# Performance work log

Hardware: AMD Instinct MI355X
Metric: run time of the kernel (lower is better)

## Reference

```python
import jax, jax.numpy as jnp
import numpy as np

TOP_K = 5
EPS = 1e-12

def _l2norm(x, axis=-1):
    n = jnp.sqrt(jnp.sum(x * x, axis=axis, keepdims=True))
    return x / jnp.maximum(n, EPS)

def setup_inputs() -> dict:
    key = jax.random.key(0)
    ks = jax.random.split(key, 6)
    B, S, D, N = 16, 2048, 512, 200000
    return {
        "hidden_states": jax.random.normal(ks[0], (B, S, D), dtype=jnp.float32),
        "doc_embeddings": jax.random.normal(ks[1], (N, D), dtype=jnp.float32),
        "W_q": jax.random.normal(ks[2], (D, D), dtype=jnp.float32) * 0.02,
        "b_q": jnp.zeros((D,), dtype=jnp.float32),
        "W_gate": jax.random.normal(ks[3], (D, 2 * D), dtype=jnp.float32) * 0.02,
        "b_gate": jnp.zeros((D,), dtype=jnp.float32),
    }

def reference(hidden_states, doc_embeddings, W_q, b_q, W_gate, b_gate):
    B, S, D = hidden_states.shape
    # set_doc_embeddings: cosine metric normalizes doc table once
    docs = _l2norm(doc_embeddings, axis=1)          # [N, D]
    # forward: mean-pool query, linear encode
    query = hidden_states.mean(axis=1)              # [B, D]
    query = query @ W_q.T + b_q                     # torch Linear: x @ W^T + b
    # cosine similarity scan over full corpus
    q = _l2norm(query, axis=1)                      # [B, D]
    scores_full = q @ docs.T                        # [B, N]  (memory-bound scan)
    top_scores, indices = jax.lax.top_k(scores_full, TOP_K)  # [B, K], [B, K]
    # fuse context (gate method)
    retrieved = docs[indices]                       # [B, K, D] gather
    weights = jax.nn.softmax(top_scores, axis=1)    # [B, K]
    context = jnp.einsum('bk,bkd->bd', weights, retrieved)   # [B, D]
    context_exp = jnp.broadcast_to(context[:, None, :], (B, S, D))
    combined = jnp.concatenate([hidden_states, context_exp], axis=-1)  # [B, S, 2D]
    gate = jax.nn.sigmoid(combined @ W_gate.T + b_gate)       # [B, S, D]
    fused = gate * hidden_states + (1.0 - gate) * context_exp
    return top_scores, indices, fused
```

## Files before the change

### kernel.cpp

```cpp
#include <hip/hip_runtime.h>
#include <hip/hip_bf16.h>
#include <math.h>

#define BB 16
#define SS 2048
#define DD 512
#define NDOCS 200000
#define TOPK 5
#define EPSN 1e-12f
#define NEG_INF (-3.0e38f)

#define TILE_N 128
#define KC 64
#define NCHUNK (DD / KC)
#define NBLK3 ((NDOCS + TILE_N - 1) / TILE_N)

typedef short s16x8 __attribute__((ext_vector_type(8)));
typedef float f32x4 __attribute__((ext_vector_type(4)));

__device__ __forceinline__ short f2bf(float f) {
    __bf16 b = (__bf16)f;
    short s;
    __builtin_memcpy(&s, &b, 2);
    return s;
}

__device__ __forceinline__ void gload_lds16(const void* g, void* l) {
    __builtin_amdgcn_global_load_lds(
        (const __attribute__((address_space(1))) void*)g,
        (__attribute__((address_space(3))) void*)l, 16, 0, 0);
}

__global__ __launch_bounds__(128) void k1_mean_partial(
    const float* __restrict__ hs, float* __restrict__ partial) {
    int b = blockIdx.y, sc = blockIdx.x;
    int t = threadIdx.x;
    const float4* src = (const float4*)(hs + (size_t)(b * SS + sc * 64) * DD);
    float4 acc = {0.f, 0.f, 0.f, 0.f};
    for (int s = 0; s < 64; ++s) {
        float4 v = src[(size_t)s * 128 + t];
        acc.x += v.x; acc.y += v.y; acc.z += v.z; acc.w += v.w;
    }
    ((float4*)partial)[(size_t)(sc * BB + b) * 128 + t] = acc;
}

__global__ __launch_bounds__(128) void k1b_mean_reduce(
    const float* __restrict__ partial, float* __restrict__ mean) {
    int b = blockIdx.y, jc = blockIdx.x;
    int j = jc * 128 + threadIdx.x;
    float s = 0.f;
    for (int c = 0; c < 32; ++c) s += partial[(size_t)(c * BB + b) * DD + j];
    mean[(size_t)b * DD + j] = s * (1.0f / 2048.0f);
}

__global__ __launch_bounds__(256) void k2a_q_gemv(
    const float* __restrict__ mean, const float* __restrict__ Wq,
    const float* __restrict__ bq, float* __restrict__ qtmp) {
    int b = blockIdx.y, jc = blockIdx.x;
    int t = threadIdx.x;
    int r = t >> 4, c = t & 15;
    int row = jc * 16 + r;
    const float4* wr = (const float4*)(Wq + (size_t)row * DD);
    const float4* mv = (const float4*)(mean + (size_t)b * DD);
    float acc = 0.f;
#pragma unroll
    for (int it = 0; it < 8; ++it) {
        int k4 = c + it * 16;
        float4 w = wr[k4], m = mv[k4];
        acc = fmaf(w.x, m.x, acc); acc = fmaf(w.y, m.y, acc);
        acc = fmaf(w.z, m.z, acc); acc = fmaf(w.w, m.w, acc);
    }
#pragma unroll
    for (int m = 1; m < 16; m <<= 1) acc += __shfl_xor(acc, m);
    if (c == 0) qtmp[(size_t)b * DD + row] = acc + bq[row];
}

__global__ __launch_bounds__(256) void k2b_q_norm(
    const float* __restrict__ qtmp, float* __restrict__ qv) {
    int b = blockIdx.x, t = threadIdx.x;
    __shared__ float red[4];
    float a0 = qtmp[(size_t)b * DD + t];
    float a1 = qtmp[(size_t)b * DD + t + 256];
    float ss = a0 * a0 + a1 * a1;
#pragma unroll
    for (int m = 1; m < 64; m <<= 1) ss += __shfl_xor(ss, m);
    if ((t & 63) == 0) red[t >> 6] = ss;
    __syncthreads();
    float inv = 1.0f / fmaxf(sqrtf(red[0] + red[1] + red[2] + red[3]), EPSN);
    qv[(size_t)b * DD + t] = a0 * inv;
    qv[(size_t)b * DD + t + 256] = a1 * inv;
}

__global__ __launch_bounds__(256) void k3_scores(
    const float* __restrict__ docs, const float* __restrict__ qv,
    float* __restrict__ cand_s, int* __restrict__ cand_i) {
    __shared__ float4 Et[2][TILE_N * 16];

    int t = threadIdx.x;
    int w = t >> 6, lane = t & 63;
    int ln = lane & 15, bg = lane >> 4;
    int blk = blockIdx.x;
    long tileBase = (long)blk * TILE_N;

    const float4* q4 = (const float4*)qv;

    auto stage = [&](int c, int buf) {
#pragma unroll
        for (int j = 0; j < 8; ++j) {
            int u = ((w * 8 + j) << 6) + lane;
            int n = u >> 4, slot = u & 15;
            int k4src = slot ^ (n & 15);
            long row = tileBase + n;
            if (row > NDOCS - 1) row = NDOCS - 1;
            const float* g = docs + row * (long)DD + c * KC + k4src * 4;
            gload_lds16(g, (void*)&Et[buf][(w * 8 + j) * 64]);
        }
    };

    float acc[2][4];
    float nrm[2];
#pragma unroll
    for (int i = 0; i < 2; ++i) {
        nrm[i] = 0.f;
#pragma unroll
        for (int j = 0; j < 4; ++j) acc[i][j] = 0.f;
    }

    stage(0, 0);
    for (int c = 0; c < NCHUNK; ++c) {
        __syncthreads();
        if (c + 1 < NCHUNK) stage(c + 1, (c + 1) & 1);
        const float4* Eb = &Et[c & 1][0];
        int c16 = c * 16;
#pragma unroll
        for (int k4 = 0; k4 < 16; ++k4) {
            float4 q0 = q4[(bg * 4 + 0) * 128 + c16 + k4];
            float4 q1 = q4[(bg * 4 + 1) * 128 + c16 + k4];
            float4 q2 = q4[(bg * 4 + 2) * 128 + c16 + k4];
            float4 q3 = q4[(bg * 4 + 3) * 128 + c16 + k4];
#pragma unroll
            for (int i = 0; i < 2; ++i) {
                int n = (w << 5) + ln + (i << 4);
                float4 e = Eb[(n << 4) + (k4 ^ (n & 15))];
                nrm[i]    = fmaf(e.x, e.x, fmaf(e.y, e.y, fmaf(e.z, e.z, fmaf(e.w, e.w, nrm[i]))));
                acc[i][0] = fmaf(e.x, q0.x, fmaf(e.y, q0.y, fmaf(e.z, q0.z, fmaf(e.w, q0.w, acc[i][0]))));
                acc[i][1] = fmaf(e.x, q1.x, fmaf(e.y, q1.y, fmaf(e.z, q1.z, fmaf(e.w, q1.w, acc[i][1]))));
                acc[i][2] = fmaf(e.x, q2.x, fmaf(e.y, q2.y, fmaf(e.z, q2.z, fmaf(e.w, q2.w, acc[i][2]))));
                acc[i][3] = fmaf(e.x, q3.x, fmaf(e.y, q3.y, fmaf(e.z, q3.z, fmaf(e.w, q3.w, acc[i][3]))));
            }
        }
    }

    float* Sb = (float*)&Et[0][0];
    __syncthreads();
#pragma unroll
    for (int i = 0; i < 2; ++i) {
        int n = (w << 5) + ln + (i << 4);
        float inv = 1.0f / fmaxf(sqrtf(nrm[i]), EPSN);
#pragma unroll
        for (int j = 0; j < 4; ++j)
            Sb[(bg * 4 + j) * TILE_N + n] = acc[i][j] * inv;
    }
    __syncthreads();

    for (int jj = 0; jj < 4; ++jj) {
        int b = w * 4 + jj;
        float v[2]; int nn[2];
#pragma unroll
        for (int m = 0; m < 2; ++m) {
            int n = lane + m * 64;
            nn[m] = n;
            v[m] = (tileBase + n < NDOCS) ? Sb[b * TILE_N + n] : NEG_INF;
        }
        for (int r = 0; r < TOPK; ++r) {
            float bv = v[0]; int bi = nn[0];
            if (v[1] > bv || (v[1] == bv && nn[1] < bi)) { bv = v[1]; bi = nn[1]; }
#pragma unroll
            for (int mm = 1; mm < 64; mm <<= 1) {
                float ov = __shfl_xor(bv, mm);
                int   oi = __shfl_xor(bi, mm);
                if (ov > bv || (ov == bv && oi < bi)) { bv = ov; bi = oi; }
            }
            if (lane == 0) {
                cand_s[((long)blk * BB + b) * TOPK + r] = bv;
                cand_i[((long)blk * BB + b) * TOPK + r] = (int)(tileBase + bi);
            }
#pragma unroll
            for (int m = 0; m < 2; ++m)
                if (nn[m] == bi) v[m] = NEG_INF;
        }
    }
}

__global__ __launch_bounds__(256) void k4a_topk_ctx(
    const float* __restrict__ docs, const float* __restrict__ cand_s,
    const int* __restrict__ cand_i, float* __restrict__ ctx,
    float* __restrict__ outp) {
    int b = blockIdx.x, t = threadIdx.x;
    __shared__ float sv[256];
    __shared__ int   si[256];
    __shared__ float topv[TOPK];
    __shared__ int   topi[TOPK];
    __shared__ float red[4];
    __shared__ float nrm5[TOPK];
    __shared__ float wts[TOPK];

    float lv[TOPK]; int li[TOPK];
#pragma unroll
    for (int r = 0; r < TOPK; ++r) { lv[r] = NEG_INF; li[r] = 0x7fffffff; }

    for (int j = t; j < NBLK3 * TOPK; j += 256) {
        int blk = j / TOPK, r = j - blk * TOPK;
        float s = cand_s[(long)blk * (BB * TOPK) + b * TOPK + r];
        int  di = cand_i[(long)blk * (BB * TOPK) + b * TOPK + r];
        if (s > lv[TOPK - 1] || (s == lv[TOPK - 1] && di < li[TOPK - 1])) {
            lv[TOPK - 1] = s; li[TOPK - 1] = di;
#pragma unroll
            for (int k = TOPK - 1; k > 0; --k) {
                if (lv[k] > lv[k - 1] || (lv[k] == lv[k - 1] && li[k] < li[k - 1])) {
                    float tv = lv[k]; lv[k] = lv[k - 1]; lv[k - 1] = tv;
                    int   ti = li[k]; li[k] = li[k - 1]; li[k - 1] = ti;
                }
            }
        }
    }

    int p = 0;
    for (int r = 0; r < TOPK; ++r) {
        float hv = (p < TOPK) ? lv[p] : NEG_INF;
        int   hi = (p < TOPK) ? li[p] : 0x7fffffff;
        sv[t] = hv; si[t] = hi;
        __syncthreads();
        for (int off = 128; off > 0; off >>= 1) {
            if (t < off) {
                float ov = sv[t + off]; int oi = si[t + off];
                if (ov > sv[t] || (ov == sv[t] && oi < si[t])) { sv[t] = ov; si[t] = oi; }
            }
            __syncthreads();
        }
        if (t == 0) { topv[r] = sv[0]; topi[r] = si[0]; }
        __syncthreads();
        if (hv == topv[r] && hi == topi[r]) ++p;
        __syncthreads();
    }

    for (int r = 0; r < TOPK; ++r) {
        const float* dr = docs + (size_t)topi[r] * DD;
        float s2 = dr[t] * dr[t] + dr[t + 256] * dr[t + 256];
#pragma unroll
        for (int m = 1; m < 64; m <<= 1) s2 += __shfl_xor(s2, m);
        if ((t & 63) == 0) red[t >> 6] = s2;
        __syncthreads();
        if (t == 0) nrm5[r] = sqrtf(red[0] + red[1] + red[2] + red[3]);
        __syncthreads();
    }

    if (t == 0) {
        float m = topv[0];
        float e[TOPK], s = 0.f;
#pragma unroll
        for (int r = 0; r < TOPK; ++r) { e[r] = expf(topv[r] - m); s += e[r]; }
#pragma unroll
        for (int r = 0; r < TOPK; ++r) wts[r] = e[r] / s;
    }
    __syncthreads();

    for (int j = t; j < DD; j += 256) {
        float c = 0.f;
#pragma unroll
        for (int r = 0; r < TOPK; ++r)
            c += wts[r] * docs[(size_t)topi[r] * DD + j] / fmaxf(nrm5[r], EPSN);
        ctx[(size_t)b * DD + j] = c;
    }

    if (t < TOPK) {
        outp[b * TOPK + t] = topv[t];
        outp[BB * TOPK + b * TOPK + t] = (float)topi[t];
    }
}

__global__ __launch_bounds__(256) void k4b_ctxb_gemv(
    const float* __restrict__ ctx, const float* __restrict__ Wg,
    const float* __restrict__ bgt, float* __restrict__ ctxb) {
    int b = blockIdx.y, jc = blockIdx.x;
    int t = threadIdx.x;
    int r = t >> 4, c = t & 15;
    int row = jc * 16 + r;
    const float4* wr = (const float4*)(Wg + (size_t)row * (2 * DD) + DD);
    const float4* mv = (const float4*)(ctx + (size_t)b * DD);
    float acc = 0.f;
#pragma unroll
    for (int it = 0; it < 8; ++it) {
        int k4 = c + it * 16;
        float4 w = wr[k4], m = mv[k4];
        acc = fmaf(w.x, m.x, acc); acc = fmaf(w.y, m.y, acc);
        acc = fmaf(w.z, m.z, acc); acc = fmaf(w.w, m.w, acc);
    }
#pragma unroll
    for (int m = 1; m < 16; m <<= 1) acc += __shfl_xor(acc, m);
    if (c == 0) ctxb[(size_t)b * DD + row] = acc + bgt[row];
}

#define BK 32
__global__ __launch_bounds__(512, 2) void k5_gemm_fused(
    const float* __restrict__ hs, const float* __restrict__ Wg,
    const float* __restrict__ ctx, const float* __restrict__ ctxb,
    float* __restrict__ outF) {
    __shared__ short At[128][BK];
    __shared__ short Bt[512][BK];
    __shared__ float ctxLds[DD];
    __shared__ float ctxbLds[DD];

    int bm = blockIdx.x;
    int t = threadIdx.x;
    int wv = t >> 6, lane = t & 63, ln = lane & 15, kg = lane >> 4;
    int wm = (wv >> 2) * 64, wn = (wv & 3) * 128;
    int bbatch = bm >> 4;

    ctxLds[t]  = ctx[(size_t)bbatch * DD + t];
    ctxbLds[t] = ctxb[(size_t)bbatch * DD + t];

    float4 pf[5][2];
    auto gload = [&](int kt) {
        {
            const float* src = hs + (size_t)(bm * 128 + (t >> 2)) * DD + kt * BK + (t & 3) * 8;
            pf[0][0] = ((const float4*)src)[0];
            pf[0][1] = ((const float4*)src)[1];
        }
#pragma unroll
        for (int i = 0; i < 4; ++i) {
            int u = t + i * 512;
            const float* src = Wg + (size_t)(u >> 2) * (2 * DD) + kt * BK + (u & 3) * 8;
            pf[1 + i][0] = ((const float4*)src)[0];
            pf[1 + i][1] = ((const float4*)src)[1];
        }
    };
    auto cvt1 = [&](float4 lo, float4 hi) {
        s16x8 cv;
        cv[0] = f2bf(lo.x); cv[1] = f2bf(lo.y); cv[2] = f2bf(lo.z); cv[3] = f2bf(lo.w);
        cv[4] = f2bf(hi.x); cv[5] = f2bf(hi.y); cv[6] = f2bf(hi.z); cv[7] = f2bf(hi.w);
        return cv;
    };
    auto cvtwrite = [&]() {
        {
            int row = t >> 2, slot = t & 3;
            int sl = slot ^ ((row >> 1) & 3);
            *(s16x8*)(&At[row][sl * 8]) = cvt1(pf[0][0], pf[0][1]);
        }
#pragma unroll
        for (int i = 0; i < 4; ++i) {
            int u = t + i * 512;
            int row = u >> 2, slot = u & 3;
            int sl = slot ^ ((row >> 1) & 3);
            *(s16x8*)(&Bt[row][sl * 8]) = cvt1(pf[1 + i][0], pf[1 + i][1]);
        }
    };

    f32x4 accv[4][8];
#pragma unroll
    for (int i = 0; i < 4; ++i)
#pragma unroll
        for (int j = 0; j < 8; ++j) accv[i][j] = (f32x4){0.f, 0.f, 0.f, 0.f};

    gload(0);
    for (int kt = 0; kt < DD / BK; ++kt) {
        __syncthreads();
        cvtwrite();
        if (kt + 1 < DD / BK) gload(kt + 1);
        __syncthreads();
        s16x8 af[4], bfr[8];
#pragma unroll
        for (int mi = 0; mi < 4; ++mi) {
            int row = wm + mi * 16 + ln;
            int sl = kg ^ ((row >> 1) & 3);
            af[mi] = *(const s16x8*)&At[row][sl * 8];
        }
#pragma unroll
        for (int nj = 0; nj < 8; ++nj) {
            int row = wn + nj * 16 + ln;
            int sl = kg ^ ((row >> 1) & 3);
            bfr[nj] = *(const s16x8*)&Bt[row][sl * 8];
        }
#pragma unroll
        for (int mi = 0; mi < 4; ++mi)
#pragma unroll
            for (int nj = 0; nj < 8; ++nj)
                accv[mi][nj] = __builtin_amdgcn_mfma_f32_16x16x32_bf16(
                    af[mi], bfr[nj], accv[mi][nj], 0, 0, 0);
    }

#pragma unroll
    for (int mi = 0; mi < 4; ++mi)
#pragma unroll
        for (int nj = 0; nj < 8; ++nj)
#pragma unroll
            for (int r = 0; r < 4; ++r) {
                int ri = wm + mi * 16 + kg * 4 + r;
                int ci = wn + nj * 16 + ln;
                size_t grow = (size_t)bm * 128 + ri;
                float logit = accv[mi][nj][r] + ctxbLds[ci];
                float g = __builtin_amdgcn_rcpf(1.0f + __expf(-logit));
                float h = hs[grow * DD + ci];
                float cx = ctxLds[ci];
                outF[grow * DD + ci] = g * h + (1.0f - g) * cx;
            }
}

extern "C" void kernel_launch(void* const* d_in, const int* in_sizes, int n_in,
                              void* d_out, int out_size, void* d_ws, size_t ws_size,
                              hipStream_t stream) {
    const float* hs   = (const float*)d_in[0];
    const float* docs = (const float*)d_in[1];
    const float* Wq   = (const float*)d_in[2];
    const float* bq   = (const float*)d_in[3];
    const float* Wg   = (const float*)d_in[4];
    const float* bgt  = (const float*)d_in[5];
    float* outp = (float*)d_out;
    float* ws = (float*)d_ws;

    float* partial = ws;
    float* mean    = partial + 32 * BB * DD;
    float* qtmp    = mean + BB * DD;
    float* qv      = qtmp + BB * DD;
    float* ctx     = qv + BB * DD;
    float* ctxb    = ctx + BB * DD;
    float* cand_s  = ctxb + BB * DD;
    int*   cand_i  = (int*)(cand_s + NBLK3 * BB * TOPK);

    k1_mean_partial<<<dim3(32, BB), 128, 0, stream>>>(hs, partial);
    k1b_mean_reduce<<<dim3(4, BB), 128, 0, stream>>>(partial, mean);
    k2a_q_gemv<<<dim3(32, BB), 256, 0, stream>>>(mean, Wq, bq, qtmp);
    k2b_q_norm<<<BB, 256, 0, stream>>>(qtmp, qv);
    k3_scores<<<NBLK3, 256, 0, stream>>>(docs, qv, cand_s, cand_i);
    k4a_topk_ctx<<<BB, 256, 0, stream>>>(docs, cand_s, cand_i, ctx, outp);
    k4b_ctxb_gemv<<<dim3(32, BB), 256, 0, stream>>>(ctx, Wg, bgt, ctxb);
    k5_gemm_fused<<<256, 512, 0, stream>>>(hs, Wg, ctx, ctxb,
                                           outp + 2 * BB * TOPK);
}
```

Baseline: 309.2 us.

## Compute doc scores and norms with split-bf16 MFMA instead of fp32 FMA

Replaces the fp32 FMA dot-product loop in the corpus scan with bf16 MFMA, splitting each fp32 value into hi and lo bf16 parts to approximate fp32 accuracy (three cross products for scores, two for norms). A new kernel pre-splits the normalized query into swizzled bf16 hi/lo arrays, which are loaded into LDS once per block, and the K chunk is halved to fit. The aim is to take the compute bottleneck off the scan so it becomes memory-bound. The cost is a small precision loss that could change top-k ties, plus conversion ALU work per element.

```diff
diff --git a/kernel.cpp b/kernel.cpp
--- a/kernel.cpp
+++ b/kernel.cpp
@@ -11,7 +11,7 @@
 #define NEG_INF (-3.0e38f)
 
 #define TILE_N 128
-#define KC 64
+#define KC 32
 #define NCHUNK (DD / KC)
 #define NBLK3 ((NDOCS + TILE_N - 1) / TILE_N)
 
@@ -91,75 +91,107 @@
     qv[(size_t)b * DD + t + 256] = a1 * inv;
 }
 
+__global__ __launch_bounds__(256) void k2c_qsplit(
+    const float* __restrict__ qv, short* __restrict__ qsplit) {
+    int b = blockIdx.x, t = threadIdx.x;
+#pragma unroll
+    for (int kk = 0; kk < 2; ++kk) {
+        int k = t + kk * 256;
+        float f = qv[(size_t)b * DD + k];
+        unsigned u = __float_as_uint(f);
+        short hi = (short)(u >> 16);
+        float r = f - __uint_as_float(u & 0xFFFF0000u);
+        short lo = f2bf(r);
+        int slot = k >> 3, j = k & 7;
+        int off = b * 512 + ((slot ^ (b & 7)) << 3) + j;
+        qsplit[off] = hi;
+        qsplit[8192 + off] = lo;
+    }
+}
+
 __global__ __launch_bounds__(256) void k3_scores(
-    const float* __restrict__ docs, const float* __restrict__ qv,
+    const float* __restrict__ docs, const short* __restrict__ qsplit,
     float* __restrict__ cand_s, int* __restrict__ cand_i) {
-    __shared__ float4 Et[2][TILE_N * 16];
+    __shared__ float4 Et[2][TILE_N * 8];
+    __shared__ short qS[2 * 8192];
 
     int t = threadIdx.x;
     int w = t >> 6, lane = t & 63;
-    int ln = lane & 15, bg = lane >> 4;
+    int bq = lane & 15, kg = lane >> 4;
     int blk = blockIdx.x;
     long tileBase = (long)blk * TILE_N;
 
-    const float4* q4 = (const float4*)qv;
+#pragma unroll
+    for (int j = 0; j < 8; ++j) {
+        int u = ((w * 8 + j) << 6) + lane;
+        gload_lds16(qsplit + (size_t)u * 8, (void*)&qS[(w * 8 + j) * 512]);
+    }
 
     auto stage = [&](int c, int buf) {
 #pragma unroll
-        for (int j = 0; j < 8; ++j) {
-            int u = ((w * 8 + j) << 6) + lane;
-            int n = u >> 4, slot = u & 15;
-            int k4src = slot ^ (n & 15);
+        for (int j = 0; j < 4; ++j) {
+            int u = ((w * 4 + j) << 6) + lane;
+            int n = u >> 3, slot = u & 7;
+            int k4src = slot ^ (n & 7);
             long row = tileBase + n;
             if (row > NDOCS - 1) row = NDOCS - 1;
-            const float* g = docs + row * (long)DD + c * KC + k4src * 4;
-            gload_lds16(g, (void*)&Et[buf][(w * 8 + j) * 64]);
+            gload_lds16(docs + row * (long)DD + c * KC + k4src * 4,
+                        (void*)&Et[buf][(w * 4 + j) * 64]);
         }
     };
 
-    float acc[2][4];
-    float nrm[2];
-#pragma unroll
-    for (int i = 0; i < 2; ++i) {
-        nrm[i] = 0.f;
-#pragma unroll
-        for (int j = 0; j < 4; ++j) acc[i][j] = 0.f;
+    f32x4 acc[2], n1[2], n2[2];
+#pragma unroll
+    for (int f = 0; f < 2; ++f) {
+        acc[f] = (f32x4){0.f, 0.f, 0.f, 0.f};
+        n1[f]  = (f32x4){0.f, 0.f, 0.f, 0.f};
+        n2[f]  = (f32x4){0.f, 0.f, 0.f, 0.f};
     }
 
     stage(0, 0);
     for (int c = 0; c < NCHUNK; ++c) {
         __syncthreads();
         if (c + 1 < NCHUNK) stage(c + 1, (c + 1) & 1);
+
+        int qphys = ((c * 4 + kg) ^ (bq & 7)) << 3;
+        s16x8 qh = *(const s16x8*)&qS[bq * 512 + qphys];
+        s16x8 ql = *(const s16x8*)&qS[8192 + bq * 512 + qphys];
+
         const float4* Eb = &Et[c & 1][0];
-        int c16 = c * 16;
-#pragma unroll
-        for (int k4 = 0; k4 < 16; ++k4) {
-            float4 q0 = q4[(bg * 4 + 0) * 128 + c16 + k4];
-            float4 q1 = q4[(bg * 4 + 1) * 128 + c16 + k4];
-            float4 q2 = q4[(bg * 4 + 2) * 128 + c16 + k4];
-            float4 q3 = q4[(bg * 4 + 3) * 128 + c16 + k4];
-#pragma unroll
-            for (int i = 0; i < 2; ++i) {
-                int n = (w << 5) + ln + (i << 4);
-                float4 e = Eb[(n << 4) + (k4 ^ (n & 15))];
-                nrm[i]    = fmaf(e.x, e.x, fmaf(e.y, e.y, fmaf(e.z, e.z, fmaf(e.w, e.w, nrm[i]))));
-                acc[i][0] = fmaf(e.x, q0.x, fmaf(e.y, q0.y, fmaf(e.z, q0.z, fmaf(e.w, q0.w, acc[i][0]))));
-                acc[i][1] = fmaf(e.x, q1.x, fmaf(e.y, q1.y, fmaf(e.z, q1.z, fmaf(e.w, q1.w, acc[i][1]))));
-                acc[i][2] = fmaf(e.x, q2.x, fmaf(e.y, q2.y, fmaf(e.z, q2.z, fmaf(e.w, q2.w, acc[i][2]))));
-                acc[i][3] = fmaf(e.x, q3.x, fmaf(e.y, q3.y, fmaf(e.z, q3.z, fmaf(e.w, q3.w, acc[i][3]))));
-            }
+#pragma unroll
+        for (int f = 0; f < 2; ++f) {
+            int d = (w << 5) + (f << 4) + bq;
+            int base = d << 3;
+            float4 e0 = Eb[base + ((kg * 2) ^ (d & 7))];
+            float4 e1 = Eb[base + ((kg * 2 + 1) ^ (d & 7))];
+            float ef[8] = {e0.x, e0.y, e0.z, e0.w, e1.x, e1.y, e1.z, e1.w};
+            s16x8 ah, al;
+#pragma unroll
+            for (int i = 0; i < 8; ++i) {
+                unsigned u = __float_as_uint(ef[i]);
+                ah[i] = (short)(u >> 16);
+                al[i] = f2bf(ef[i] - __uint_as_float(u & 0xFFFF0000u));
+            }
+            acc[f] = __builtin_amdgcn_mfma_f32_16x16x32_bf16(ah, qh, acc[f], 0, 0, 0);
+            acc[f] = __builtin_amdgcn_mfma_f32_16x16x32_bf16(ah, ql, acc[f], 0, 0, 0);
+            acc[f] = __builtin_amdgcn_mfma_f32_16x16x32_bf16(al, qh, acc[f], 0, 0, 0);
+            n1[f]  = __builtin_amdgcn_mfma_f32_16x16x32_bf16(ah, ah, n1[f], 0, 0, 0);
+            n2[f]  = __builtin_amdgcn_mfma_f32_16x16x32_bf16(ah, al, n2[f], 0, 0, 0);
         }
     }
 
     float* Sb = (float*)&Et[0][0];
-    __syncthreads();
-#pragma unroll
-    for (int i = 0; i < 2; ++i) {
-        int n = (w << 5) + ln + (i << 4);
-        float inv = 1.0f / fmaxf(sqrtf(nrm[i]), EPSN);
-#pragma unroll
-        for (int j = 0; j < 4; ++j)
-            Sb[(bg * 4 + j) * TILE_N + n] = acc[i][j] * inv;
+#pragma unroll
+    for (int f = 0; f < 2; ++f) {
+        int rd = bq & 3;
+        float nd = n1[f][rd] + 2.0f * n2[f][rd];
+        float invn = 1.0f / fmaxf(sqrtf(nd), EPSN);
+#pragma unroll
+        for (int r = 0; r < 4; ++r) {
+            float iv = __shfl(invn, kg * 20 + r);
+            int n = (w << 5) + (f << 4) + (kg << 2) + r;
+            Sb[bq * TILE_N + n] = acc[f][r] * iv;
+        }
     }
     __syncthreads();
 
@@ -426,12 +458,14 @@
     float* ctxb    = ctx + BB * DD;
     float* cand_s  = ctxb + BB * DD;
     int*   cand_i  = (int*)(cand_s + NBLK3 * BB * TOPK);
+    short* qsplit  = (short*)(cand_i + NBLK3 * BB * TOPK);
 
     k1_mean_partial<<<dim3(32, BB), 128, 0, stream>>>(hs, partial);
     k1b_mean_reduce<<<dim3(4, BB), 128, 0, stream>>>(partial, mean);
     k2a_q_gemv<<<dim3(32, BB), 256, 0, stream>>>(mean, Wq, bq, qtmp);
     k2b_q_norm<<<BB, 256, 0, stream>>>(qtmp, qv);
-    k3_scores<<<NBLK3, 256, 0, stream>>>(docs, qv, cand_s, cand_i);
+    k2c_qsplit<<<BB, 256, 0, stream>>>(qv, qsplit);
+    k3_scores<<<NBLK3, 256, 0, stream>>>(docs, qsplit, cand_s, cand_i);
     k4a_topk_ctx<<<BB, 256, 0, stream>>>(docs, cand_s, cand_i, ctx, outp);
     k4b_ctxb_gemv<<<dim3(32, BB), 256, 0, stream>>>(ctx, Wg, bgt, ctxb);
     k5_gemm_fused<<<256, 512, 0, stream>>>(hs, Wg, ctx, ctxb,
```

New measurement: 256.0 us. -17.2%, faster.

## Restructure doc scoring so each lane streams one doc row against LDS-resident queries

Applied to the files above, without the earlier changes.

The scoring kernel now loads all 16 normalized queries into shared memory once per block, and each lane handles one whole document row. It reads the row directly from global memory with register double-buffering and keeps 16 accumulators, so the docs tile no longer goes through LDS staging. Per-warp top-5 candidates over 64 docs replace per-block top-5 over 128, which doubles the candidate count that the merge kernel must scan. The risk is poor coalescing, since each lane strides a separate 2KB row, plus heavy LDS broadcast reads of the queries and higher register pressure under launch_bounds(256,1).

```diff
diff --git a/kernel.cpp b/kernel.cpp
--- a/kernel.cpp
+++ b/kernel.cpp
@@ -10,10 +10,8 @@
 #define EPSN 1e-12f
 #define NEG_INF (-3.0e38f)
 
-#define TILE_N 128
-#define KC 64
-#define NCHUNK (DD / KC)
-#define NBLK3 ((NDOCS + TILE_N - 1) / TILE_N)
+#define NT3 (NDOCS / 64)
+#define NB3 782
 
 typedef short s16x8 __attribute__((ext_vector_type(8)));
 typedef float f32x4 __attribute__((ext_vector_type(4)));
@@ -91,103 +89,81 @@
     qv[(size_t)b * DD + t + 256] = a1 * inv;
 }
 
-__global__ __launch_bounds__(256) void k3_scores(
+__global__ __launch_bounds__(256, 1) void k3_scores(
     const float* __restrict__ docs, const float* __restrict__ qv,
     float* __restrict__ cand_s, int* __restrict__ cand_i) {
-    __shared__ float4 Et[2][TILE_N * 16];
+    __shared__ float qS[BB * DD];
 
     int t = threadIdx.x;
     int w = t >> 6, lane = t & 63;
-    int ln = lane & 15, bg = lane >> 4;
-    int blk = blockIdx.x;
-    long tileBase = (long)blk * TILE_N;
-
-    const float4* q4 = (const float4*)qv;
-
-    auto stage = [&](int c, int buf) {
-#pragma unroll
-        for (int j = 0; j < 8; ++j) {
-            int u = ((w * 8 + j) << 6) + lane;
-            int n = u >> 4, slot = u & 15;
-            int k4src = slot ^ (n & 15);
-            long row = tileBase + n;
-            if (row > NDOCS - 1) row = NDOCS - 1;
-            const float* g = docs + row * (long)DD + c * KC + k4src * 4;
-            gload_lds16(g, (void*)&Et[buf][(w * 8 + j) * 64]);
-        }
-    };
-
-    float acc[2][4];
-    float nrm[2];
-#pragma unroll
-    for (int i = 0; i < 2; ++i) {
-        nrm[i] = 0.f;
-#pragma unroll
-        for (int j = 0; j < 4; ++j) acc[i][j] = 0.f;
-    }
-
-    stage(0, 0);
-    for (int c = 0; c < NCHUNK; ++c) {
-        __syncthreads();
-        if (c + 1 < NCHUNK) stage(c + 1, (c + 1) & 1);
-        const float4* Eb = &Et[c & 1][0];
-        int c16 = c * 16;
-#pragma unroll
-        for (int k4 = 0; k4 < 16; ++k4) {
-            float4 q0 = q4[(bg * 4 + 0) * 128 + c16 + k4];
-            float4 q1 = q4[(bg * 4 + 1) * 128 + c16 + k4];
-            float4 q2 = q4[(bg * 4 + 2) * 128 + c16 + k4];
-            float4 q3 = q4[(bg * 4 + 3) * 128 + c16 + k4];
-#pragma unroll
-            for (int i = 0; i < 2; ++i) {
-                int n = (w << 5) + ln + (i << 4);
-                float4 e = Eb[(n << 4) + (k4 ^ (n & 15))];
-                nrm[i]    = fmaf(e.x, e.x, fmaf(e.y, e.y, fmaf(e.z, e.z, fmaf(e.w, e.w, nrm[i]))));
-                acc[i][0] = fmaf(e.x, q0.x, fmaf(e.y, q0.y, fmaf(e.z, q0.z, fmaf(e.w, q0.w, acc[i][0]))));
-                acc[i][1] = fmaf(e.x, q1.x, fmaf(e.y, q1.y, fmaf(e.z, q1.z, fmaf(e.w, q1.w, acc[i][1]))));
-                acc[i][2] = fmaf(e.x, q2.x, fmaf(e.y, q2.y, fmaf(e.z, q2.z, fmaf(e.w, q2.w, acc[i][2]))));
-                acc[i][3] = fmaf(e.x, q3.x, fmaf(e.y, q3.y, fmaf(e.z, q3.z, fmaf(e.w, q3.w, acc[i][3]))));
-            }
-        }
-    }
-
-    float* Sb = (float*)&Et[0][0];
+
+#pragma unroll
+    for (int jj = 0; jj < 8; ++jj) {
+        int u = ((w * 8 + jj) << 6) + lane;
+        gload_lds16(qv + (size_t)u * 4, (void*)&qS[(w * 8 + jj) * 256]);
+    }
     __syncthreads();
-#pragma unroll
-    for (int i = 0; i < 2; ++i) {
-        int n = (w << 5) + ln + (i << 4);
-        float inv = 1.0f / fmaxf(sqrtf(nrm[i]), EPSN);
-#pragma unroll
-        for (int j = 0; j < 4; ++j)
-            Sb[(bg * 4 + j) * TILE_N + n] = acc[i][j] * inv;
-    }
-    __syncthreads();
-
-    for (int jj = 0; jj < 4; ++jj) {
-        int b = w * 4 + jj;
-        float v[2]; int nn[2];
-#pragma unroll
-        for (int m = 0; m < 2; ++m) {
-            int n = lane + m * 64;
-            nn[m] = n;
-            v[m] = (tileBase + n < NDOCS) ? Sb[b * TILE_N + n] : NEG_INF;
-        }
+
+    int gw = blockIdx.x * 4 + w;
+    if (gw >= NT3) return;
+
+    const float4* dp = (const float4*)(docs + (size_t)(gw * 64 + lane) * DD);
+    const float4* q4 = (const float4*)qS;
+
+    float acc[BB];
+#pragma unroll
+    for (int b = 0; b < BB; ++b) acc[b] = 0.f;
+    float nrm = 0.f;
+
+    float4 cur[4], nxt[4];
+#pragma unroll
+    for (int i = 0; i < 4; ++i) cur[i] = dp[i];
+
+    for (int g = 0; g < 32; ++g) {
+        int gn = (g < 31) ? (g + 1) : 31;
+#pragma unroll
+        for (int i = 0; i < 4; ++i) nxt[i] = dp[gn * 4 + i];
+#pragma unroll
+        for (int i = 0; i < 4; ++i) {
+            float4 e = cur[i];
+            int k4 = g * 4 + i;
+            nrm = fmaf(e.x, e.x, fmaf(e.y, e.y, fmaf(e.z, e.z, fmaf(e.w, e.w, nrm))));
+#pragma unroll
+            for (int b = 0; b < BB; ++b) {
+                float4 qq = q4[b * 128 + k4];
+                acc[b] = fmaf(e.x, qq.x, fmaf(e.y, qq.y,
+                          fmaf(e.z, qq.z, fmaf(e.w, qq.w, acc[b]))));
+            }
+        }
+#pragma unroll
+        for (int i = 0; i < 4; ++i) cur[i] = nxt[i];
+    }
+
+    float invn = 1.0f / fmaxf(sqrtf(nrm), EPSN);
+    long base = (long)gw * 64;
+
+#pragma unroll 1
+    for (int b = 0; b < BB; ++b) {
+        float v = acc[b] * invn;
+        float lvv[TOPK]; int lii[TOPK];
+#pragma unroll
         for (int r = 0; r < TOPK; ++r) {
-            float bv = v[0]; int bi = nn[0];
-            if (v[1] > bv || (v[1] == bv && nn[1] < bi)) { bv = v[1]; bi = nn[1]; }
+            float bv = v; int bi = lane;
 #pragma unroll
             for (int mm = 1; mm < 64; mm <<= 1) {
                 float ov = __shfl_xor(bv, mm);
                 int   oi = __shfl_xor(bi, mm);
                 if (ov > bv || (ov == bv && oi < bi)) { bv = ov; bi = oi; }
             }
-            if (lane == 0) {
-                cand_s[((long)blk * BB + b) * TOPK + r] = bv;
-                cand_i[((long)blk * BB + b) * TOPK + r] = (int)(tileBase + bi);
-            }
-#pragma unroll
-            for (int m = 0; m < 2; ++m)
-                if (nn[m] == bi) v[m] = NEG_INF;
+            lvv[r] = bv; lii[r] = bi;
+            if (lane == bi) v = NEG_INF;
+        }
+        if (lane == 0) {
+#pragma unroll
+            for (int r = 0; r < TOPK; ++r) {
+                cand_s[((long)gw * BB + b) * TOPK + r] = lvv[r];
+                cand_i[((long)gw * BB + b) * TOPK + r] = (int)(base + lii[r]);
+            }
         }
     }
 }
@@ -209,7 +185,7 @@
 #pragma unroll
     for (int r = 0; r < TOPK; ++r) { lv[r] = NEG_INF; li[r] = 0x7fffffff; }
 
-    for (int j = t; j < NBLK3 * TOPK; j += 256) {
+    for (int j = t; j < NT3 * TOPK; j += 256) {
         int blk = j / TOPK, r = j - blk * TOPK;
         float s = cand_s[(long)blk * (BB * TOPK) + b * TOPK + r];
         int  di = cand_i[(long)blk * (BB * TOPK) + b * TOPK + r];
@@ -425,13 +401,13 @@
     float* ctx     = qv + BB * DD;
     float* ctxb    = ctx + BB * DD;
     float* cand_s  = ctxb + BB * DD;
-    int*   cand_i  = (int*)(cand_s + NBLK3 * BB * TOPK);
+    int*   cand_i  = (int*)(cand_s + (size_t)NT3 * BB * TOPK);
 
     k1_mean_partial<<<dim3(32, BB), 128, 0, stream>>>(hs, partial);
     k1b_mean_reduce<<<dim3(4, BB), 128, 0, stream>>>(partial, mean);
     k2a_q_gemv<<<dim3(32, BB), 256, 0, stream>>>(mean, Wq, bq, qtmp);
     k2b_q_norm<<<BB, 256, 0, stream>>>(qtmp, qv);
-    k3_scores<<<NBLK3, 256, 0, stream>>>(docs, qv, cand_s, cand_i);
+    k3_scores<<<NB3, 256, 0, stream>>>(docs, qv, cand_s, cand_i);
     k4a_topk_ctx<<<BB, 256, 0, stream>>>(docs, cand_s, cand_i, ctx, outp);
     k4b_ctxb_gemv<<<dim3(32, BB), 256, 0, stream>>>(ctx, Wg, bgt, ctxb);
     k5_gemm_fused<<<256, 512, 0, stream>>>(hs, Wg, ctx, ctxb,
```

Result: slower. 355.1 us (+14.9%).
